# Kernel optimization log

Hardware: AMD Instinct MI355X
Metric: run time of the kernel (lower is better)

## Reference

```python
import jax, jax.numpy as jnp
import numpy as np

L, B, N, D, H = 4, 4, 2048, 512, 8
HD = D // H  # head dim 64
EPS = 1e-5

def setup_inputs() -> dict:
    key = jax.random.key(0)
    ks = jax.random.split(key, 8)
    s = 0.02  # init scale for weights
    f32 = jnp.float32
    return {
        "x": jax.random.normal(ks[0], (B, N, D), f32),
        "Wq": jax.random.normal(ks[1], (L, D, D), f32) * s,
        "Wk": jax.random.normal(ks[2], (L, D, D), f32) * s,
        "Wv": jax.random.normal(ks[3], (L, D, D), f32) * s,
        "Wo": jax.random.normal(ks[4], (L, D, D), f32) * s,
        "bo": jnp.zeros((L, D), f32),
        "ln1_g": jnp.ones((L, D), f32),
        "ln1_b": jnp.zeros((L, D), f32),
        "W1": jax.random.normal(ks[5], (L, D, D), f32) * s,
        "b1": jnp.zeros((L, D), f32),
        "W2": jax.random.normal(ks[6], (L, D, D), f32) * s,
        "b2": jnp.zeros((L, D), f32),
        "ln2_g": jnp.ones((L, D), f32),
        "ln2_b": jnp.zeros((L, D), f32),
    }

def _layernorm(x, g, b):
    mu = jnp.mean(x, axis=-1, keepdims=True)
    var = jnp.mean(jnp.square(x - mu), axis=-1, keepdims=True)
    return (x - mu) * jax.lax.rsqrt(var + EPS) * g + b

def reference(x, Wq, Wk, Wv, Wo, bo, ln1_g, ln1_b, W1, b1, W2, b2, ln2_g, ln2_b):
    scale = D ** -0.5  # dim1 == dim on the cfg=None path

    def layer(h, p):
        wq, wk, wv, wo, bo_, g1, bb1, w1, bh1, w2, bh2, g2, bb2 = p
        # --- Residual(PreNorm(Attention)) ---
        y = _layernorm(h, g1, bb1)
        def split_heads(t):  # [B,N,D] -> [B,H,N,HD]
            return t.reshape(B, N, H, HD).transpose(0, 2, 1, 3)
        q = split_heads(y @ wq)
        k = split_heads(y @ wk)
        v = split_heads(y @ wv)
        dots = jnp.einsum('bhid,bhjd->bhij', q, k) * scale
        attn = jax.nn.softmax(dots, axis=-1)
        o = jnp.einsum('bhij,bhjd->bhid', attn, v)
        o = o.transpose(0, 2, 1, 3).reshape(B, N, D)
        h = h + o @ wo + bo_
        # --- Residual(PreNorm(FeedForward)) ---
        y = _layernorm(h, g2, bb2)
        y = jax.nn.gelu(y @ w1 + bh1, approximate=False)
        h = h + y @ w2 + bh2
        return h, None

    params = (Wq, Wk, Wv, Wo, bo, ln1_g, ln1_b, W1, b1, W2, b2, ln2_g, ln2_b)
    out, _ = jax.lax.scan(layer, x, params)
    return out
```

## Files before the change

kernel.cpp:

```cpp
#include <hip/hip_runtime.h>
#include <hip/hip_bf16.h>


typedef __bf16 bf16x8 __attribute__((ext_vector_type(8)));
typedef float f32x4 __attribute__((ext_vector_type(4)));
typedef unsigned int u32x4 __attribute__((ext_vector_type(4)));
typedef unsigned int u32x2 __attribute__((ext_vector_type(2)));
typedef unsigned short u16;

__device__ __forceinline__ u16 f2b(float f) {
  unsigned int u; __builtin_memcpy(&u, &f, 4);
  u += 0x7fffu + ((u >> 16) & 1u);
  return (u16)(u >> 16);
}
__device__ __forceinline__ bf16x8 ld8(const u16* p) {
  u32x4 t = *(const u32x4*)p;
  bf16x8 r; __builtin_memcpy(&r, &t, 16); return r;
}
__device__ __forceinline__ unsigned pkhi(float a, float b) {
  unsigned ua, ub; __builtin_memcpy(&ua, &a, 4); __builtin_memcpy(&ub, &b, 4);
  return __builtin_amdgcn_perm(ua, ub, 0x07060302u);
}

#define GLL(gp, lp) __builtin_amdgcn_global_load_lds( \
    (const __attribute__((address_space(1))) void*)(gp), \
    (__attribute__((address_space(3))) void*)(lp), 16, 0, 0)

__device__ __forceinline__ int swz(int r) { return (r + (r >> 2)) & 3; }

__global__ __launch_bounds__(256) void tr_all_k(
    const float* __restrict__ Wq, const float* __restrict__ Wk,
    const float* __restrict__ Wv, const float* __restrict__ Wo,
    const float* __restrict__ W1, const float* __restrict__ W2,
    u16* __restrict__ wtqkv, u16* __restrict__ wto,
    u16* __restrict__ wt1, u16* __restrict__ wt2) {
  __shared__ float t[32][33];
  int tx = threadIdx.x, ty = threadIdx.y;
  int z = blockIdx.z, which = z >> 2, l = z & 3;
  const float* in;
  u16* out;
  switch (which) {
    case 0: in = Wq; out = wtqkv + l * 786432; break;
    case 1: in = Wk; out = wtqkv + l * 786432 + 262144; break;
    case 2: in = Wv; out = wtqkv + l * 786432 + 524288; break;
    case 3: in = Wo; out = wto + l * 262144; break;
    case 4: in = W1; out = wt1 + l * 262144; break;
    default: in = W2; out = wt2 + l * 262144; break;
  }
  int k0 = blockIdx.y * 32, n0 = blockIdx.x * 32;
  const float* ip = in + l * 262144;
#pragma unroll
  for (int i = 0; i < 4; i++)
    t[ty + i * 8][tx] = ip[(k0 + ty + i * 8) * 512 + n0 + tx];
  __syncthreads();
#pragma unroll
  for (int i = 0; i < 4; i++)
    out[(n0 + ty + i * 8) * 512 + k0 + tx] = f2b(t[tx][ty + i * 8]);
}

__global__ __launch_bounds__(256) void ln_k(const float* __restrict__ h,
                                            const float* __restrict__ gg,
                                            const float* __restrict__ bb,
                                            u16* __restrict__ y) {
  int tid = threadIdx.x, wave = tid >> 6, lane = tid & 63;
  int tok = blockIdx.x * 4 + wave;
  const float* hp = h + (size_t)tok * 512 + lane * 8;
  float x[8];
  *(float4*)&x[0] = *(const float4*)hp;
  *(float4*)&x[4] = *(const float4*)(hp + 4);
  float s = 0.f, ss = 0.f;
#pragma unroll
  for (int i = 0; i < 8; i++) { s += x[i]; ss += x[i] * x[i]; }
#pragma unroll
  for (int off = 1; off < 64; off <<= 1) {
    s += __shfl_xor(s, off, 64);
    ss += __shfl_xor(ss, off, 64);
  }
  float mean = s * (1.0f / 512.0f);
  float var = ss * (1.0f / 512.0f) - mean * mean;
  float rstd = rsqrtf(var + 1e-5f);
  u32x4 ov;
#pragma unroll
  for (int i = 0; i < 4; i++) {
    int d0 = lane * 8 + i * 2;
    float y0 = (x[i * 2]     - mean) * rstd * gg[d0]     + bb[d0];
    float y1 = (x[i * 2 + 1] - mean) * rstd * gg[d0 + 1] + bb[d0 + 1];
    ov[i] = (unsigned)f2b(y0) | ((unsigned)f2b(y1) << 16);
  }
  *(u32x4*)&y[(size_t)tok * 512 + lane * 8] = ov;
}

enum { EPI_RES = 1, EPI_GELU = 2 };

template <int EPI>
__global__ __launch_bounds__(512, 4) void gemm2_k(
    const u16* __restrict__ A, const u16* __restrict__ Bt,
    const float* __restrict__ bias, u16* __restrict__ out0,
    const float* __restrict__ hin, float* __restrict__ hout,
    float* __restrict__ fout) {
  __shared__ __align__(16) u16 As[2][64 * 32];
  __shared__ __align__(16) u16 Bs[2][128 * 32];
  const int tid = threadIdx.x;
  const int wave = tid >> 6, lane = tid & 63;
  const int quad = lane >> 4, l16 = lane & 15;
  const int wm = wave >> 2, wn = wave & 3;
  const int m0 = blockIdx.x * 64;
  const int n0 = blockIdx.y * 128;
  const int mb = m0 + wm * 32, nb = n0 + wn * 32;

  float hr[2][2][4];
  if constexpr (EPI == EPI_RES) {
#pragma unroll
    for (int mi = 0; mi < 2; ++mi)
#pragma unroll
      for (int ni = 0; ni < 2; ++ni) {
        int r0 = mb + mi * 16 + quad * 4, c = nb + ni * 16 + l16;
#pragma unroll
        for (int g = 0; g < 4; ++g)
          hr[mi][ni][g] = hin[(size_t)(r0 + g) * 512 + c];
      }
  }

  f32x4 acc[2][2];
#pragma unroll
  for (int i = 0; i < 2; i++)
#pragma unroll
    for (int j = 0; j < 2; j++) acc[i][j] = f32x4{0.f, 0.f, 0.f, 0.f};

  const int rowA = (tid & 255) >> 2, cgA = (tid & 3) ^ swz(rowA);
  const size_t agl = (size_t)(m0 + rowA) * 512 + cgA * 8;
  const int rowB = tid >> 2, cgB = (tid & 3) ^ swz(rowB);
  const size_t bgl = (size_t)(n0 + rowB) * 512 + cgB * 8;

  int kbA[2], kbB[2];
#pragma unroll
  for (int mi = 0; mi < 2; ++mi) {
    int r = wm * 32 + mi * 16 + l16;
    kbA[mi] = r * 32 + (quad ^ swz(r)) * 8;
  }
#pragma unroll
  for (int ni = 0; ni < 2; ++ni) {
    int r = wn * 32 + ni * 16 + l16;
    kbB[ni] = r * 32 + (quad ^ swz(r)) * 8;
  }

  if (tid < 256) GLL(A + agl, &As[0][(wave * 64) * 8]);
  GLL(Bt + bgl, &Bs[0][(wave * 64) * 8]);

#pragma unroll 2
  for (int kt = 0; kt < 16; ++kt) {
    __syncthreads();
    const u16* AsB = As[kt & 1];
    const u16* BsB = Bs[kt & 1];
    if (kt + 1 < 16) {
      u16* AsN = (u16*)As[(kt & 1) ^ 1];
      u16* BsN = (u16*)Bs[(kt & 1) ^ 1];
      const int k1 = (kt + 1) * 32;
      if (tid < 256) GLL(A + agl + k1, AsN + (wave * 64) * 8);
      GLL(Bt + bgl + k1, BsN + (wave * 64) * 8);
    }

    bf16x8 af[2], bf_[2];
#pragma unroll
    for (int mi = 0; mi < 2; ++mi) af[mi] = ld8(AsB + kbA[mi]);
#pragma unroll
    for (int ni = 0; ni < 2; ++ni) bf_[ni] = ld8(BsB + kbB[ni]);
#pragma unroll
    for (int mi = 0; mi < 2; ++mi)
#pragma unroll
      for (int ni = 0; ni < 2; ++ni)
        acc[mi][ni] = __builtin_amdgcn_mfma_f32_16x16x32_bf16(
            af[mi], bf_[ni], acc[mi][ni], 0, 0, 0);
  }

#pragma unroll
  for (int mi = 0; mi < 2; ++mi) {
#pragma unroll
    for (int ni = 0; ni < 2; ++ni) {
      f32x4 a = acc[mi][ni];
      int r0 = mb + mi * 16 + quad * 4;
      int c = nb + ni * 16 + l16;
      float bi = bias[c];
      if constexpr (EPI == EPI_RES) {
#pragma unroll
        for (int g = 0; g < 4; ++g) {
          float v = hr[mi][ni][g] + a[g] + bi;
          hout[(size_t)(r0 + g) * 512 + c] = v;
          if (fout) fout[(size_t)(r0 + g) * 512 + c] = v;
        }
      } else {
#pragma unroll
        for (int g = 0; g < 4; ++g) {
          float t = a[g] + bi;
          float gl = 0.5f * t * (1.0f + erff(t * 0.70710678118654752f));
          out0[(size_t)(r0 + g) * 512 + c] = f2b(gl);
        }
      }
    }
  }
}

__global__ __launch_bounds__(256, 6) void gemm_qkv_k(
    const u16* __restrict__ A, const u16* __restrict__ Bt,
    u16* __restrict__ outq, u16* __restrict__ outk, u16* __restrict__ outvt) {
  __shared__ __align__(16) u16 As[2][64 * 32];
  __shared__ __align__(16) u16 Bs[2][128 * 32];
  const int tid = threadIdx.x;
  const int wave = tid >> 6, lane = tid & 63;
  const int quad = lane >> 4, l16 = lane & 15;
  const int wm = wave >> 1, wn = wave & 1;
  const int m0 = blockIdx.x * 64;
  const int n0 = blockIdx.y * 128;
  const int mb = m0 + wm * 32, nb = n0 + wn * 64;

  f32x4 acc[2][4];
#pragma unroll
  for (int i = 0; i < 2; i++)
#pragma unroll
    for (int j = 0; j < 4; j++) acc[i][j] = f32x4{0.f, 0.f, 0.f, 0.f};

  const int sA0 = wave * 64 + lane;
  const int rowA = sA0 >> 2, cgA = (sA0 & 3) ^ swz(rowA);
  const size_t agl = (size_t)(m0 + rowA) * 512 + cgA * 8;
  int rowB[2], cgB[2];
#pragma unroll
  for (int rnd = 0; rnd < 2; ++rnd) {
    int s = rnd * 256 + sA0;
    rowB[rnd] = s >> 2;
    cgB[rnd] = (s & 3) ^ swz(rowB[rnd]);
  }
  const size_t bgl0 = (size_t)(n0 + rowB[0]) * 512 + cgB[0] * 8;
  const size_t bgl1 = (size_t)(n0 + rowB[1]) * 512 + cgB[1] * 8;

  int kbA[2], kbB[4];
#pragma unroll
  for (int mi = 0; mi < 2; ++mi) {
    int r = wm * 32 + mi * 16 + l16;
    kbA[mi] = r * 32 + (quad ^ swz(r)) * 8;
  }
#pragma unroll
  for (int ni = 0; ni < 4; ++ni) {
    int r = wn * 64 + ni * 16 + l16;
    kbB[ni] = r * 32 + (quad ^ swz(r)) * 8;
  }

  GLL(A + agl, &As[0][(wave * 64) * 8]);
  GLL(Bt + bgl0, &Bs[0][(wave * 64) * 8]);
  GLL(Bt + bgl1, &Bs[0][(256 + wave * 64) * 8]);

#pragma unroll 2
  for (int kt = 0; kt < 16; ++kt) {
    __syncthreads();
    const u16* AsB = As[kt & 1];
    const u16* BsB = Bs[kt & 1];
    if (kt + 1 < 16) {
      u16* AsN = (u16*)As[(kt & 1) ^ 1];
      u16* BsN = (u16*)Bs[(kt & 1) ^ 1];
      const int k1 = (kt + 1) * 32;
      GLL(A + agl + k1, AsN + (wave * 64) * 8);
      GLL(Bt + bgl0 + k1, BsN + (wave * 64) * 8);
      GLL(Bt + bgl1 + k1, BsN + (256 + wave * 64) * 8);
    }

    bf16x8 af[2], bf_[4];
#pragma unroll
    for (int mi = 0; mi < 2; ++mi) af[mi] = ld8(AsB + kbA[mi]);
#pragma unroll
    for (int ni = 0; ni < 4; ++ni) bf_[ni] = ld8(BsB + kbB[ni]);
#pragma unroll
    for (int mi = 0; mi < 2; ++mi)
#pragma unroll
      for (int ni = 0; ni < 4; ++ni)
        acc[mi][ni] = __builtin_amdgcn_mfma_f32_16x16x32_bf16(
            af[mi], bf_[ni], acc[mi][ni], 0, 0, 0);
  }

#pragma unroll
  for (int mi = 0; mi < 2; ++mi) {
#pragma unroll
    for (int ni = 0; ni < 4; ++ni) {
      f32x4 a = acc[mi][ni];
      int r0 = mb + mi * 16 + quad * 4;
      int c = nb + ni * 16 + l16;
      if (c < 512) {
        const float C2 = 0.06375871506958306f;
#pragma unroll
        for (int g = 0; g < 4; ++g) outq[(size_t)(r0 + g) * 512 + c] = f2b(a[g] * C2);
      } else if (c < 1024) {
#pragma unroll
        for (int g = 0; g < 4; ++g) outk[(size_t)(r0 + g) * 512 + (c - 512)] = f2b(a[g]);
      } else {
        int cv = c - 1024, hh = cv >> 6, dd = cv & 63;
        int bb = r0 >> 11, nt = r0 & 2047;
        u32x2 pk;
        pk[0] = (unsigned)f2b(a[0]) | ((unsigned)f2b(a[1]) << 16);
        pk[1] = (unsigned)f2b(a[2]) | ((unsigned)f2b(a[3]) << 16);
        *(u32x2*)&outvt[((size_t)(bb * 8 + hh) * 64 + dd) * 2048 + nt] = pk;
      }
    }
  }
}

__global__ __launch_bounds__(256, 4) void attn_k(const u16* __restrict__ q,
                                                 const u16* __restrict__ k,
                                                 const u16* __restrict__ vt,
                                                 u16* __restrict__ o) {
  __shared__ __align__(16) u16 Ks[2][64 * 64];
  __shared__ __align__(16) u16 Vs[2][64 * 64];
  __shared__ float Lr[4][32];
  const int tid = threadIdx.x, wave = tid >> 6, lane = tid & 63;
  const int quad = lane >> 4, l16 = lane & 15;
  const int swl = l16 & 7;
  const int qh2 = wave & 1, kvs = wave >> 1;
  const int bh = blockIdx.x, b = bh >> 3, h = bh & 7;
  const int qt0 = blockIdx.y * 64;

  const u16* qpb = q + (size_t)(b * 2048 + qt0 + qh2 * 32) * 512 + h * 64;
  bf16x8 aq[2][2];
#pragma unroll
  for (int qt = 0; qt < 2; ++qt) {
    const u16* qp = qpb + (size_t)(qt * 16 + l16) * 512;
    aq[qt][0] = ld8(qp + quad * 8);
    aq[qt][1] = ld8(qp + 32 + quad * 8);
  }

  const u16* kp = k + (size_t)b * 2048 * 512 + h * 64;
  const u16* vp = vt + (size_t)bh * 64 * 2048;

  const int srow = lane >> 3, schk = lane & 7, sgc = schk ^ srow;
  const int krow0 = wave * 8 + srow;
  const size_t kgl0 = (size_t)krow0 * 512 + sgc * 8;
  const size_t kgl1 = (size_t)(krow0 + 32) * 512 + sgc * 8;
  const size_t vgl0 = (size_t)krow0 * 2048 + sgc * 8;
  const size_t vgl1 = (size_t)(krow0 + 32) * 2048 + sgc * 8;

  int kb[2][2];
#pragma unroll
  for (int t = 0; t < 2; ++t) {
    kb[t][0] = (kvs * 32 + t * 16 + l16) * 64 + ((quad)     ^ swl) * 8;
    kb[t][1] = (kvs * 32 + t * 16 + l16) * 64 + ((4 + quad) ^ swl) * 8;
  }
  const int vblo = l16 * 64 + (((kvs << 2) + (quad >> 1)) ^ swl) * 8 + (quad & 1) * 4;
  const int vbhi = l16 * 64 + (((kvs << 2) + 2 + (quad >> 1)) ^ swl) * 8 + (quad & 1) * 4;

  f32x4 oacc[4][2];
#pragma unroll
  for (int i = 0; i < 4; i++)
#pragma unroll
    for (int j = 0; j < 2; j++) oacc[i][j] = f32x4{0.f, 0.f, 0.f, 0.f};
  f32x4 lsacc[2];
  lsacc[0] = f32x4{0.f, 0.f, 0.f, 0.f};
  lsacc[1] = f32x4{0.f, 0.f, 0.f, 0.f};

  u32x4 onesw;
  onesw[0] = 0x3F803F80u; onesw[1] = 0x3F803F80u;
  onesw[2] = 0x3F803F80u; onesw[3] = 0x3F803F80u;
  bf16x8 onesf; __builtin_memcpy(&onesf, &onesw, 16);

  GLL(kp + kgl0, &Ks[0][(wave * 8) * 64]);
  GLL(kp + kgl1, &Ks[0][(32 + wave * 8) * 64]);
  GLL(vp + vgl0, &Vs[0][(wave * 8) * 64]);
  GLL(vp + vgl1, &Vs[0][(32 + wave * 8) * 64]);

#pragma unroll 2
  for (int kt = 0; kt < 32; ++kt) {
    __syncthreads();
    const u16* KsB = Ks[kt & 1];
    const u16* VsB = Vs[kt & 1];
    if (kt + 1 < 32) {
      u16* KsN = (u16*)Ks[(kt & 1) ^ 1];
      u16* VsN = (u16*)Vs[(kt & 1) ^ 1];
      const u16* kpn = kp + (size_t)(kt + 1) * 32768;
      const u16* vpn = vp + (size_t)(kt + 1) * 64;
      GLL(kpn + kgl0, KsN + (wave * 8) * 64);
      GLL(kpn + kgl1, KsN + (32 + wave * 8) * 64);
      GLL(vpn + vgl0, VsN + (wave * 8) * 64);
      GLL(vpn + vgl1, VsN + (32 + wave * 8) * 64);
    }

    bf16x8 kf[2][2];
#pragma unroll
    for (int t = 0; t < 2; ++t) {
      kf[t][0] = ld8(KsB + kb[t][0]);
      kf[t][1] = ld8(KsB + kb[t][1]);
    }
    f32x4 sa[2][2];
    __builtin_amdgcn_s_setprio(1);
#pragma unroll
    for (int t = 0; t < 2; ++t)
#pragma unroll
      for (int qt = 0; qt < 2; ++qt) {
        f32x4 z = f32x4{0.f, 0.f, 0.f, 0.f};
        z = __builtin_amdgcn_mfma_f32_16x16x32_bf16(kf[t][0], aq[qt][0], z, 0, 0, 0);
        z = __builtin_amdgcn_mfma_f32_16x16x32_bf16(kf[t][1], aq[qt][1], z, 0, 0, 0);
        sa[t][qt] = z;
      }
    __builtin_amdgcn_s_setprio(0);

    u32x4 pw[2];
#pragma unroll
    for (int t = 0; t < 2; ++t)
#pragma unroll
      for (int qt = 0; qt < 2; ++qt) {
        float p0 = __builtin_amdgcn_exp2f(sa[t][qt][0]);
        float p1 = __builtin_amdgcn_exp2f(sa[t][qt][1]);
        float p2 = __builtin_amdgcn_exp2f(sa[t][qt][2]);
        float p3 = __builtin_amdgcn_exp2f(sa[t][qt][3]);
        pw[qt][t * 2]     = pkhi(p1, p0);
        pw[qt][t * 2 + 1] = pkhi(p3, p2);
      }
    bf16x8 pf[2];
    __builtin_memcpy(&pf[0], &pw[0], 16);
    __builtin_memcpy(&pf[1], &pw[1], 16);

    __builtin_amdgcn_s_setprio(1);
#pragma unroll
    for (int dt = 0; dt < 4; ++dt) {
      u32x2 lo = *(const u32x2*)(VsB + vblo + dt * 1024);
      u32x2 hi = *(const u32x2*)(VsB + vbhi + dt * 1024);
      u32x4 w;
      w[0] = lo[0]; w[1] = lo[1]; w[2] = hi[0]; w[3] = hi[1];
      bf16x8 av; __builtin_memcpy(&av, &w, 16);
#pragma unroll
      for (int qt = 0; qt < 2; ++qt)
        oacc[dt][qt] = __builtin_amdgcn_mfma_f32_16x16x32_bf16(
            av, pf[qt], oacc[dt][qt], 0, 0, 0);
    }
#pragma unroll
    for (int qt = 0; qt < 2; ++qt)
      lsacc[qt] = __builtin_amdgcn_mfma_f32_16x16x32_bf16(
          onesf, pf[qt], lsacc[qt], 0, 0, 0);
    __builtin_amdgcn_s_setprio(0);
  }

  if (quad == 0) {
#pragma unroll
    for (int qt = 0; qt < 2; ++qt) Lr[wave][qt * 16 + l16] = lsacc[qt][0];
  }
  __syncthreads();

  float* R = (float*)&Ks[0][0];
  const int l7 = lane & 7;
  if (wave >= 2) {
    float* Rw = R + (wave - 2) * 2048;
#pragma unroll
    for (int dt = 0; dt < 4; ++dt)
#pragma unroll
      for (int qt = 0; qt < 2; ++qt) {
        int s = (dt * 2 + qt) ^ l7;
        *(f32x4*)&Rw[lane * 32 + s * 4] = oacc[dt][qt];
      }
  }
  __syncthreads();
  if (wave < 2) {
    float* Rw = R + wave * 2048;
    float inv[2];
#pragma unroll
    for (int qt = 0; qt < 2; ++qt)
      inv[qt] = 1.0f / (Lr[wave][qt * 16 + l16] + Lr[wave + 2][qt * 16 + l16]);
#pragma unroll
    for (int dt = 0; dt < 4; ++dt)
#pragma unroll
      for (int qt = 0; qt < 2; ++qt) {
        int s = (dt * 2 + qt) ^ l7;
        f32x4 v = *(f32x4*)&Rw[lane * 32 + s * 4];
        float i4 = inv[qt];
        float o0 = (oacc[dt][qt][0] + v[0]) * i4;
        float o1 = (oacc[dt][qt][1] + v[1]) * i4;
        float o2 = (oacc[dt][qt][2] + v[2]) * i4;
        float o3 = (oacc[dt][qt][3] + v[3]) * i4;
        u16* op = o + (size_t)(b * 2048 + qt0 + wave * 32 + qt * 16 + l16) * 512 +
                  h * 64 + dt * 16 + quad * 4;
        u32x2 pk;
        pk[0] = (unsigned)f2b(o0) | ((unsigned)f2b(o1) << 16);
        pk[1] = (unsigned)f2b(o2) | ((unsigned)f2b(o3) << 16);
        *(u32x2*)op = pk;
      }
  }
}

extern "C" void kernel_launch(void* const* d_in, const int* in_sizes, int n_in,
                              void* d_out, int out_size, void* d_ws,
                              size_t ws_size, hipStream_t stream) {
  const float* x   = (const float*)d_in[0];
  const float* Wq  = (const float*)d_in[1];
  const float* Wk  = (const float*)d_in[2];
  const float* Wv  = (const float*)d_in[3];
  const float* Wo  = (const float*)d_in[4];
  const float* bo  = (const float*)d_in[5];
  const float* g1  = (const float*)d_in[6];
  const float* bg1 = (const float*)d_in[7];
  const float* W1  = (const float*)d_in[8];
  const float* b1  = (const float*)d_in[9];
  const float* W2  = (const float*)d_in[10];
  const float* b2  = (const float*)d_in[11];
  const float* g2  = (const float*)d_in[12];
  const float* bg2 = (const float*)d_in[13];

  char* ws = (char*)d_ws;
  float* h    = (float*)ws;
  u16* yb     = (u16*)(ws + (16ll << 20));
  u16* qb     = (u16*)(ws + (24ll << 20));
  u16* kb     = (u16*)(ws + (32ll << 20));
  u16* vtb    = (u16*)(ws + (40ll << 20));
  u16* ob     = (u16*)(ws + (48ll << 20));
  u16* wtqkv  = (u16*)(ws + (56ll << 20));
  u16* wto    = (u16*)(ws + (62ll << 20));
  u16* wt1    = (u16*)(ws + (64ll << 20));
  u16* wt2    = (u16*)(ws + (66ll << 20));

  tr_all_k<<<dim3(16, 16, 24), dim3(32, 8), 0, stream>>>(
      Wq, Wk, Wv, Wo, W1, W2, wtqkv, wto, wt1, wt2);

  for (int l = 0; l < 4; ++l) {
    const float* hsrc = (l == 0) ? x : h;
    ln_k<<<2048, 256, 0, stream>>>(hsrc, g1 + l * 512, bg1 + l * 512, yb);
    gemm_qkv_k<<<dim3(128, 12), 256, 0, stream>>>(
        yb, wtqkv + l * 786432, qb, kb, vtb);
    attn_k<<<dim3(32, 32), 256, 0, stream>>>(qb, kb, vtb, ob);
    gemm2_k<EPI_RES><<<dim3(128, 4), 512, 0, stream>>>(
        ob, wto + l * 262144, bo + l * 512, nullptr, hsrc, h, nullptr);
    ln_k<<<2048, 256, 0, stream>>>(h, g2 + l * 512, bg2 + l * 512, yb);
    gemm2_k<EPI_GELU><<<dim3(128, 4), 512, 0, stream>>>(
        yb, wt1 + l * 262144, b1 + l * 512, qb, nullptr, nullptr, nullptr);
    gemm2_k<EPI_RES><<<dim3(128, 4), 512, 0, stream>>>(
        qb, wt2 + l * 262144, b2 + l * 512, nullptr, h, h,
        (l == 3) ? (float*)d_out : nullptr);
  }
}
```

Baseline: 589.5 us.

## Double GEMM K-tile to 64 and widen QKV GEMM to 512 threads

Both GEMM kernels now stage 64-wide K slices in LDS instead of 32, which halves the number of k-iterations and barriers and changes the swizzle to an 8-group XOR. The QKV projection kernel moves from 256 to 512 threads per block with 8 waves, each computing a 32x32 sub-tile instead of 32x64. This cuts per-wave accumulator registers and spreads the loads over more threads. LDS use per block doubles, which may limit how many blocks fit on a CU.

```diff
diff --git a/kernel.cpp b/kernel.cpp
--- a/kernel.cpp
+++ b/kernel.cpp
@@ -98,8 +98,8 @@
     const float* __restrict__ bias, u16* __restrict__ out0,
     const float* __restrict__ hin, float* __restrict__ hout,
     float* __restrict__ fout) {
-  __shared__ __align__(16) u16 As[2][64 * 32];
-  __shared__ __align__(16) u16 Bs[2][128 * 32];
+  __shared__ __align__(16) u16 As[2][64 * 64];
+  __shared__ __align__(16) u16 Bs[2][128 * 64];
   const int tid = threadIdx.x;
   const int wave = tid >> 6, lane = tid & 63;
   const int quad = lane >> 4, l16 = lane & 15;
@@ -127,50 +127,66 @@
 #pragma unroll
     for (int j = 0; j < 2; j++) acc[i][j] = f32x4{0.f, 0.f, 0.f, 0.f};
 
-  const int rowA = (tid & 255) >> 2, cgA = (tid & 3) ^ swz(rowA);
+  const int rowA = tid >> 3, cgA = (tid & 7) ^ (rowA & 7);
   const size_t agl = (size_t)(m0 + rowA) * 512 + cgA * 8;
-  const int rowB = tid >> 2, cgB = (tid & 3) ^ swz(rowB);
-  const size_t bgl = (size_t)(n0 + rowB) * 512 + cgB * 8;
-
-  int kbA[2], kbB[2];
+  int rowB[2], cgB[2];
+#pragma unroll
+  for (int rnd = 0; rnd < 2; ++rnd) {
+    int s = rnd * 512 + tid;
+    rowB[rnd] = s >> 3;
+    cgB[rnd] = (tid & 7) ^ (rowB[rnd] & 7);
+  }
+  const size_t bgl0 = (size_t)(n0 + rowB[0]) * 512 + cgB[0] * 8;
+  const size_t bgl1 = (size_t)(n0 + rowB[1]) * 512 + cgB[1] * 8;
+
+  int kbA[2][2], kbB[2][2];
 #pragma unroll
   for (int mi = 0; mi < 2; ++mi) {
     int r = wm * 32 + mi * 16 + l16;
-    kbA[mi] = r * 32 + (quad ^ swz(r)) * 8;
+#pragma unroll
+    for (int ks = 0; ks < 2; ++ks)
+      kbA[mi][ks] = r * 64 + ((ks * 4 + quad) ^ (r & 7)) * 8;
   }
 #pragma unroll
   for (int ni = 0; ni < 2; ++ni) {
     int r = wn * 32 + ni * 16 + l16;
-    kbB[ni] = r * 32 + (quad ^ swz(r)) * 8;
-  }
-
-  if (tid < 256) GLL(A + agl, &As[0][(wave * 64) * 8]);
-  GLL(Bt + bgl, &Bs[0][(wave * 64) * 8]);
+#pragma unroll
+    for (int ks = 0; ks < 2; ++ks)
+      kbB[ni][ks] = r * 64 + ((ks * 4 + quad) ^ (r & 7)) * 8;
+  }
+
+  GLL(A + agl, &As[0][(wave * 64) * 8]);
+  GLL(Bt + bgl0, &Bs[0][(wave * 64) * 8]);
+  GLL(Bt + bgl1, &Bs[0][(512 + wave * 64) * 8]);
 
 #pragma unroll 2
-  for (int kt = 0; kt < 16; ++kt) {
+  for (int kt = 0; kt < 8; ++kt) {
     __syncthreads();
     const u16* AsB = As[kt & 1];
     const u16* BsB = Bs[kt & 1];
-    if (kt + 1 < 16) {
+    if (kt + 1 < 8) {
       u16* AsN = (u16*)As[(kt & 1) ^ 1];
       u16* BsN = (u16*)Bs[(kt & 1) ^ 1];
-      const int k1 = (kt + 1) * 32;
-      if (tid < 256) GLL(A + agl + k1, AsN + (wave * 64) * 8);
-      GLL(Bt + bgl + k1, BsN + (wave * 64) * 8);
-    }
-
-    bf16x8 af[2], bf_[2];
-#pragma unroll
-    for (int mi = 0; mi < 2; ++mi) af[mi] = ld8(AsB + kbA[mi]);
-#pragma unroll
-    for (int ni = 0; ni < 2; ++ni) bf_[ni] = ld8(BsB + kbB[ni]);
-#pragma unroll
-    for (int mi = 0; mi < 2; ++mi)
-#pragma unroll
-      for (int ni = 0; ni < 2; ++ni)
-        acc[mi][ni] = __builtin_amdgcn_mfma_f32_16x16x32_bf16(
-            af[mi], bf_[ni], acc[mi][ni], 0, 0, 0);
+      const int k1 = (kt + 1) * 64;
+      GLL(A + agl + k1, AsN + (wave * 64) * 8);
+      GLL(Bt + bgl0 + k1, BsN + (wave * 64) * 8);
+      GLL(Bt + bgl1 + k1, BsN + (512 + wave * 64) * 8);
+    }
+
+#pragma unroll
+    for (int ks = 0; ks < 2; ++ks) {
+      bf16x8 af[2], bf_[2];
+#pragma unroll
+      for (int mi = 0; mi < 2; ++mi) af[mi] = ld8(AsB + kbA[mi][ks]);
+#pragma unroll
+      for (int ni = 0; ni < 2; ++ni) bf_[ni] = ld8(BsB + kbB[ni][ks]);
+#pragma unroll
+      for (int mi = 0; mi < 2; ++mi)
+#pragma unroll
+        for (int ni = 0; ni < 2; ++ni)
+          acc[mi][ni] = __builtin_amdgcn_mfma_f32_16x16x32_bf16(
+              af[mi], bf_[ni], acc[mi][ni], 0, 0, 0);
+    }
   }
 
 #pragma unroll
@@ -200,85 +216,91 @@
   }
 }
 
-__global__ __launch_bounds__(256, 6) void gemm_qkv_k(
+__global__ __launch_bounds__(512, 6) void gemm_qkv_k(
     const u16* __restrict__ A, const u16* __restrict__ Bt,
     u16* __restrict__ outq, u16* __restrict__ outk, u16* __restrict__ outvt) {
-  __shared__ __align__(16) u16 As[2][64 * 32];
-  __shared__ __align__(16) u16 Bs[2][128 * 32];
+  __shared__ __align__(16) u16 As[2][64 * 64];
+  __shared__ __align__(16) u16 Bs[2][128 * 64];
   const int tid = threadIdx.x;
   const int wave = tid >> 6, lane = tid & 63;
   const int quad = lane >> 4, l16 = lane & 15;
-  const int wm = wave >> 1, wn = wave & 1;
+  const int wm = wave >> 2, wn = wave & 3;
   const int m0 = blockIdx.x * 64;
   const int n0 = blockIdx.y * 128;
-  const int mb = m0 + wm * 32, nb = n0 + wn * 64;
-
-  f32x4 acc[2][4];
+  const int mb = m0 + wm * 32, nb = n0 + wn * 32;
+
+  f32x4 acc[2][2];
 #pragma unroll
   for (int i = 0; i < 2; i++)
 #pragma unroll
-    for (int j = 0; j < 4; j++) acc[i][j] = f32x4{0.f, 0.f, 0.f, 0.f};
-
-  const int sA0 = wave * 64 + lane;
-  const int rowA = sA0 >> 2, cgA = (sA0 & 3) ^ swz(rowA);
+    for (int j = 0; j < 2; j++) acc[i][j] = f32x4{0.f, 0.f, 0.f, 0.f};
+
+  const int rowA = tid >> 3, cgA = (tid & 7) ^ (rowA & 7);
   const size_t agl = (size_t)(m0 + rowA) * 512 + cgA * 8;
   int rowB[2], cgB[2];
 #pragma unroll
   for (int rnd = 0; rnd < 2; ++rnd) {
-    int s = rnd * 256 + sA0;
-    rowB[rnd] = s >> 2;
-    cgB[rnd] = (s & 3) ^ swz(rowB[rnd]);
+    int s = rnd * 512 + tid;
+    rowB[rnd] = s >> 3;
+    cgB[rnd] = (tid & 7) ^ (rowB[rnd] & 7);
   }
   const size_t bgl0 = (size_t)(n0 + rowB[0]) * 512 + cgB[0] * 8;
   const size_t bgl1 = (size_t)(n0 + rowB[1]) * 512 + cgB[1] * 8;
 
-  int kbA[2], kbB[4];
+  int kbA[2][2], kbB[2][2];
 #pragma unroll
   for (int mi = 0; mi < 2; ++mi) {
     int r = wm * 32 + mi * 16 + l16;
-    kbA[mi] = r * 32 + (quad ^ swz(r)) * 8;
-  }
-#pragma unroll
-  for (int ni = 0; ni < 4; ++ni) {
-    int r = wn * 64 + ni * 16 + l16;
-    kbB[ni] = r * 32 + (quad ^ swz(r)) * 8;
+#pragma unroll
+    for (int ks = 0; ks < 2; ++ks)
+      kbA[mi][ks] = r * 64 + ((ks * 4 + quad) ^ (r & 7)) * 8;
+  }
+#pragma unroll
+  for (int ni = 0; ni < 2; ++ni) {
+    int r = wn * 32 + ni * 16 + l16;
+#pragma unroll
+    for (int ks = 0; ks < 2; ++ks)
+      kbB[ni][ks] = r * 64 + ((ks * 4 + quad) ^ (r & 7)) * 8;
   }
 
   GLL(A + agl, &As[0][(wave * 64) * 8]);
   GLL(Bt + bgl0, &Bs[0][(wave * 64) * 8]);
-  GLL(Bt + bgl1, &Bs[0][(256 + wave * 64) * 8]);
+  GLL(Bt + bgl1, &Bs[0][(512 + wave * 64) * 8]);
 
 #pragma unroll 2
-  for (int kt = 0; kt < 16; ++kt) {
+  for (int kt = 0; kt < 8; ++kt) {
     __syncthreads();
     const u16* AsB = As[kt & 1];
     const u16* BsB = Bs[kt & 1];
-    if (kt + 1 < 16) {
+    if (kt + 1 < 8) {
       u16* AsN = (u16*)As[(kt & 1) ^ 1];
       u16* BsN = (u16*)Bs[(kt & 1) ^ 1];
-      const int k1 = (kt + 1) * 32;
+      const int k1 = (kt + 1) * 64;
       GLL(A + agl + k1, AsN + (wave * 64) * 8);
       GLL(Bt + bgl0 + k1, BsN + (wave * 64) * 8);
-      GLL(Bt + bgl1 + k1, BsN + (256 + wave * 64) * 8);
-    }
-
-    bf16x8 af[2], bf_[4];
-#pragma unroll
-    for (int mi = 0; mi < 2; ++mi) af[mi] = ld8(AsB + kbA[mi]);
-#pragma unroll
-    for (int ni = 0; ni < 4; ++ni) bf_[ni] = ld8(BsB + kbB[ni]);
-#pragma unroll
-    for (int mi = 0; mi < 2; ++mi)
-#pragma unroll
-      for (int ni = 0; ni < 4; ++ni)
-        acc[mi][ni] = __builtin_amdgcn_mfma_f32_16x16x32_bf16(
-            af[mi], bf_[ni], acc[mi][ni], 0, 0, 0);
+      GLL(Bt + bgl1 + k1, BsN + (512 + wave * 64) * 8);
+    }
+
+#pragma unroll
+    for (int ks = 0; ks < 2; ++ks) {
+      bf16x8 af[2], bf_[2];
+#pragma unroll
+      for (int mi = 0; mi < 2; ++mi) af[mi] = ld8(AsB + kbA[mi][ks]);
+#pragma unroll
+      for (int ni = 0; ni < 2; ++ni) bf_[ni] = ld8(BsB + kbB[ni][ks]);
+#pragma unroll
+      for (int mi = 0; mi < 2; ++mi)
+#pragma unroll
+        for (int ni = 0; ni < 2; ++ni)
+          acc[mi][ni] = __builtin_amdgcn_mfma_f32_16x16x32_bf16(
+              af[mi], bf_[ni], acc[mi][ni], 0, 0, 0);
+    }
   }
 
 #pragma unroll
   for (int mi = 0; mi < 2; ++mi) {
 #pragma unroll
-    for (int ni = 0; ni < 4; ++ni) {
+    for (int ni = 0; ni < 2; ++ni) {
       f32x4 a = acc[mi][ni];
       int r0 = mb + mi * 16 + quad * 4;
       int c = nb + ni * 16 + l16;
@@ -515,7 +537,7 @@
   for (int l = 0; l < 4; ++l) {
     const float* hsrc = (l == 0) ? x : h;
     ln_k<<<2048, 256, 0, stream>>>(hsrc, g1 + l * 512, bg1 + l * 512, yb);
-    gemm_qkv_k<<<dim3(128, 12), 256, 0, stream>>>(
+    gemm_qkv_k<<<dim3(128, 12), 512, 0, stream>>>(
         yb, wtqkv + l * 786432, qb, kb, vtb);
     attn_k<<<dim3(32, 32), 256, 0, stream>>>(qb, kb, vtb, ob);
     gemm2_k<EPI_RES><<<dim3(128, 4), 512, 0, stream>>>(
```

After: 546.2 us. -7.4%, faster.
